# Performance work log

Measured on AMD Instinct MI355X. Metric: run time of the kernel, lower is better.

## Reference

```python
import jax, jax.numpy as jnp
import numpy as np

N = 100000   # n_node
D = 64       # emb_size
NNZ = 3200000
B, L = 64, 200
LAYERS = 2


def setup_inputs() -> dict:
    key = jax.random.key(0)
    ks = jax.random.split(key, 12)
    s = 1.0 / np.sqrt(D)  # reset_parameters uniform(-stdv, stdv)
    u = lambda k, shape: jax.random.uniform(k, shape, minval=-s, maxval=s, dtype=jnp.float32)
    return {
        "input": jax.random.randint(ks[0], (B, L), 0, N).astype(jnp.int32),
        "h_item_idx": jax.random.randint(ks[1], (2, NNZ), 0, N).astype(jnp.int32),
        "h_item_val": jax.random.uniform(ks[2], (NNZ,), dtype=jnp.float32),
        "h_user_idx": jax.random.randint(ks[3], (2, NNZ), 0, N).astype(jnp.int32),
        "h_user_val": jax.random.uniform(ks[4], (NNZ,), dtype=jnp.float32),
        "user_emb": u(ks[5], (N, D)),
        "w0": u(ks[6], (D, D)),
        "w1": u(ks[7], (D, D)),
        "b0": u(ks[8], (1, D)),
        "b1": u(ks[9], (1, D)),
        "att": u(ks[10], (1, D)),
        "att_m": u(ks[11], (D, D)),
    }


def _spmm(idx, val, x):
    # torch.sparse.mm(H, x) with H given as COO (rows=idx[0], cols=idx[1])
    gathered = val[:, None] * x[idx[1]]              # [nnz, D]
    return jax.ops.segment_sum(gathered, idx[0], num_segments=N)


def _l2norm(x):
    # F.normalize(x, p=2, dim=1), eps=1e-12
    n = jnp.maximum(jnp.linalg.norm(x, axis=1, keepdims=True), 1e-12)
    return x / n


def _structure_embed(h_item_idx, h_item_val, h_user_idx, h_user_val,
                     user_emb, w0, w1, b0, b1, att, att_m):
    # self_gating per channel (eval mode: no graph dropout)
    e2 = user_emb * jax.nn.sigmoid(user_emb @ w0 + b0)
    e3 = user_emb * jax.nn.sigmoid(user_emb @ w1 + b1)
    acc2, acc3 = e2, e3
    for _ in range(LAYERS):
        e2 = _spmm(h_item_idx, h_item_val, e2)
        acc2 = acc2 + _l2norm(e2)
        e3 = _spmm(h_user_idx, h_user_val, e3)
        acc3 = acc3 + _l2norm(e3)
    # channel attention over the two channel embeddings
    w_c2 = jnp.sum(att * (acc2 @ att_m), axis=1)     # [N]
    w_c3 = jnp.sum(att * (acc3 @ att_m), axis=1)     # [N]
    score = jax.nn.softmax(jnp.stack([w_c2, w_c3], axis=1), axis=-1)  # [N, 2]
    mixed = score[:, 0:1] * acc2 + score[:, 1:2] * acc3
    return mixed


def reference(input, h_item_idx, h_item_val, h_user_idx, h_user_val,
              user_emb, w0, w1, b0, b1, att, att_m):
    mask = input == 0                                 # [B, L]
    hg = _structure_embed(h_item_idx, h_item_val, h_user_idx, h_user_val,
                          user_emb, w0, w1, b0, b1, att, att_m)
    cas_seq_emb = hg[input]                           # [B, L, D]
    source_emb = cas_seq_emb[:, 0, :]                 # [B, D]
    # long-term attention: source query attends over the cascade sequence
    scores = jnp.einsum("bd,bld->bl", source_emb, cas_seq_emb) / np.sqrt(D)
    scores = jnp.where(mask, -1e9, scores)
    attw = jax.nn.softmax(scores, axis=-1)            # [B, L]
    L_cas_emb = attw[:, :, None] * cas_seq_emb        # [B, L, D]
    return (L_cas_emb, cas_seq_emb)
```

## Files before the change

### kernel.cpp

```cpp
#include <hip/hip_runtime.h>
#include <cstdint>
#include <cstddef>

typedef unsigned short ushort_t;

#define N_NODES 100000
#define D 64
#define NNZ 3200000
#define BB 64
#define LL 200
#define BSHIFT 7
#define BSIZE 128
#define NBUCK 782
#define CAP 4608
#define EPT 9
#define BM_WORDS 3200
#define BCHUNK 4096
#define BEPT 4

__device__ __forceinline__ float wave_sum(float x) {
#pragma unroll
  for (int o = 32; o; o >>= 1) x += __shfl_xor(x, o, 64);
  return x;
}
__device__ __forceinline__ float bf2f(uint32_t h) {
  return __uint_as_float(h << 16);
}
__device__ __forceinline__ uint32_t f2b(float f) {
  uint32_t u = __float_as_uint(f);
  return (u + 0x7FFFu + ((u >> 16) & 1u)) >> 16;
}

__global__ void mark_kernel(const int* __restrict__ input, uint32_t* __restrict__ bm,
                            int* __restrict__ list, int* __restrict__ nlist) {
  int t = blockIdx.x * 256 + threadIdx.x;
  if (t < BB * LL) {
    int i = input[t];
    uint32_t bit = 1u << (i & 31);
    uint32_t old = atomicOr(&bm[i >> 5], bit);
    if (!(old & bit)) {
      int p = atomicAdd(nlist, 1);
      list[p] = i;
    }
  }
}

__global__ __launch_bounds__(256) void gate_kernel(
    const float* __restrict__ u, const float* __restrict__ w0,
    const float* __restrict__ w1, const float* __restrict__ b0,
    const float* __restrict__ b1, float* __restrict__ e2, float* __restrict__ e3,
    ushort_t* __restrict__ h2, ushort_t* __restrict__ h3) {
  __shared__ float sw0[D * D];
  __shared__ float sw1[D * D];
  __shared__ float sb0[D], sb1[D];
  for (int t = threadIdx.x; t < D * D; t += 256) { sw0[t] = w0[t]; sw1[t] = w1[t]; }
  if (threadIdx.x < D) { sb0[threadIdx.x] = b0[threadIdx.x]; sb1[threadIdx.x] = b1[threadIdx.x]; }
  __syncthreads();
  int wave = (blockIdx.x * 256 + threadIdx.x) >> 6;
  int lane = threadIdx.x & 63;
  int nw = (gridDim.x * 256) >> 6;
  for (int i = wave; i < N_NODES; i += nw) {
    float uv = u[i * D + lane];
    float a0 = 0.f, a1 = 0.f;
#pragma unroll
    for (int k = 0; k < D; ++k) {
      float uk = __shfl(uv, k, 64);
      a0 = fmaf(uk, sw0[k * D + lane], a0);
      a1 = fmaf(uk, sw1[k * D + lane], a1);
    }
    a0 += sb0[lane];
    a1 += sb1[lane];
    float s0 = 1.f / (1.f + expf(-a0));
    float s1 = 1.f / (1.f + expf(-a1));
    float r2 = uv * s0, r3 = uv * s1;
    e2[i * D + lane] = r2;
    e3[i * D + lane] = r3;
    h2[i * D + lane] = (ushort_t)f2b(r2);
    h3[i * D + lane] = (ushort_t)f2b(r3);
  }
}

__global__ void init_cursor_kernel(uint32_t* __restrict__ gcursor) {
  int t = blockIdx.x * 256 + threadIdx.x;
  if (t < NBUCK) gcursor[t] = (uint32_t)t * CAP;
}

__global__ __launch_bounds__(1024) void bin_kernel(
    const int* __restrict__ dsts, const int* __restrict__ srcs,
    const float* __restrict__ val, uint32_t* __restrict__ gcursor,
    uint2* __restrict__ binned) {
  __shared__ uint2 sp[BCHUNK];
  __shared__ uint32_t hist[NBUCK];
  __shared__ uint32_t sst[NBUCK + 1];
  __shared__ uint32_t gbase[NBUCK];
  int base = blockIdx.x * BCHUNK;
  int tid = threadIdx.x;
  for (int t = tid; t < NBUCK; t += 1024) hist[t] = 0u;
  __syncthreads();
  int n = NNZ - base;
  if (n > BCHUNK) n = BCHUNK;
  uint32_t px[BEPT]; float pv[BEPT]; uint32_t pb[BEPT]; uint32_t pr[BEPT];
#pragma unroll
  for (int k = 0; k < BEPT; ++k) {
    int off = (k << 10) + tid;
    bool ok = off < n;
    int e = base + off;
    int d = ok ? dsts[e] : 0;
    int s = ok ? srcs[e] : 0;
    float v = ok ? val[e] : 0.f;
    uint32_t b = (uint32_t)d >> BSHIFT;
    pb[k] = ok ? b : 0xFFFFFFFFu;
    pr[k] = ok ? atomicAdd(&hist[b], 1u) : 0u;
    px[k] = (uint32_t)s | ((uint32_t)(d & (BSIZE - 1)) << 17);
    pv[k] = v;
  }
  __syncthreads();
  for (int t = tid; t < NBUCK; t += 1024) {
    uint32_t h = hist[t];
    gbase[t] = h ? atomicAdd(&gcursor[t], h) : 0u;
    sst[t + 1] = h;
  }
  if (tid == 0) sst[0] = 0u;
  __syncthreads();
  for (int o = 1; o < NBUCK; o <<= 1) {
    uint32_t t = 0u;
    if (tid < NBUCK && (int)(tid + 1) > o) t = sst[tid + 1 - o];
    __syncthreads();
    if (tid < NBUCK && (int)(tid + 1) > o) sst[tid + 1] += t;
    __syncthreads();
  }
#pragma unroll
  for (int k = 0; k < BEPT; ++k) {
    if (pb[k] != 0xFFFFFFFFu)
      sp[sst[pb[k]] + pr[k]] = make_uint2(px[k], __float_as_uint(pv[k]));
  }
  __syncthreads();
  for (int idx = tid; idx < n; idx += 1024) {
    int lo = 0, hi = NBUCK;
    while (hi - lo > 1) {
      int mid = (lo + hi) >> 1;
      if ((int)sst[mid] <= idx) lo = mid; else hi = mid;
    }
    uint32_t pos = gbase[lo] + ((uint32_t)idx - sst[lo]);
    if (pos < (uint32_t)(lo + 1) * CAP) {
      binned[pos] = sp[idx];
    }
  }
}

__global__ __launch_bounds__(512) void sortspmm_kernel(
    const uint32_t* __restrict__ gcursor, uint2* __restrict__ binned,
    const ushort_t* __restrict__ xin, ushort_t* __restrict__ xout,
    uint32_t* __restrict__ grow_start, uint32_t* __restrict__ grow_cnt) {
  __shared__ uint2 sp[CAP];
  __shared__ uint32_t hist[BSIZE];
  __shared__ uint32_t ssc[BSIZE];
  __shared__ uint32_t sst[BSIZE];
  int bucket = blockIdx.x, tid = threadIdx.x;
  int nodebase = bucket << BSHIFT;
  uint32_t cnt = gcursor[bucket] - (uint32_t)bucket * CAP;
  if (cnt > CAP) cnt = CAP;
  if (tid < BSIZE) hist[tid] = 0u;
  __syncthreads();
  uint2 pr[EPT]; uint32_t rk[EPT];
  const uint2* ep = binned + (size_t)bucket * CAP;
#pragma unroll
  for (int k = 0; k < EPT; ++k) {
    int e = (k << 9) + tid;
    if (e < (int)cnt) {
      pr[k] = ep[e];
      rk[k] = atomicAdd(&hist[pr[k].x >> 17], 1u);
    }
  }
  __syncthreads();
  if (tid < BSIZE) ssc[tid] = hist[tid];
  __syncthreads();
  for (int o = 1; o < BSIZE; o <<= 1) {
    uint32_t t = 0;
    if (tid < BSIZE && tid >= o) t = ssc[tid - o];
    __syncthreads();
    if (tid < BSIZE) ssc[tid] += t;
    __syncthreads();
  }
  if (tid < BSIZE) sst[tid] = ssc[tid] - hist[tid];
  __syncthreads();
#pragma unroll
  for (int k = 0; k < EPT; ++k) {
    int e = (k << 9) + tid;
    if (e < (int)cnt) sp[sst[pr[k].x >> 17] + rk[k]] = pr[k];
  }
  __syncthreads();
  for (int t = tid; t < (int)cnt; t += 512) binned[(size_t)bucket * CAP + t] = sp[t];
  int nvalid = N_NODES - nodebase;
  if (nvalid > BSIZE) nvalid = BSIZE;
  if (tid < nvalid) {
    grow_start[nodebase + tid] = (uint32_t)bucket * CAP + sst[tid];
    grow_cnt[nodebase + tid] = hist[tid];
  }
  int wave = tid >> 6, lane = tid & 63, g = lane >> 4, c = lane & 15;
  for (int r = wave; r < nvalid; r += 8) {
    uint32_t rc = hist[r], s0 = sst[r];
    float ax = 0.f, ay = 0.f, az = 0.f, aw = 0.f;
    for (uint32_t j0 = 0; j0 < rc; j0 += 32) {
      uint2 pk[8];
#pragma unroll
      for (int k = 0; k < 8; ++k) {
        uint32_t e = j0 + (uint32_t)g + (uint32_t)(k << 2);
        pk[k] = (e < rc) ? sp[s0 + e] : make_uint2(0u, 0u);
      }
      uint2 qk[8];
#pragma unroll
      for (int k = 0; k < 8; ++k) {
        uint32_t src = pk[k].x & 0x1FFFFu;
        qk[k] = ((const uint2*)(xin + (size_t)src * D))[c];
      }
#pragma unroll
      for (int k = 0; k < 8; ++k) {
        float v = __uint_as_float(pk[k].y);
        ax = fmaf(v, bf2f(qk[k].x & 0xFFFFu), ax);
        ay = fmaf(v, bf2f(qk[k].x >> 16), ay);
        az = fmaf(v, bf2f(qk[k].y & 0xFFFFu), az);
        aw = fmaf(v, bf2f(qk[k].y >> 16), aw);
      }
    }
#pragma unroll
    for (int o = 16; o <= 32; o <<= 1) {
      ax += __shfl_xor(ax, o, 64); ay += __shfl_xor(ay, o, 64);
      az += __shfl_xor(az, o, 64); aw += __shfl_xor(aw, o, 64);
    }
    if (g == 0) {
      uint32_t lo = f2b(ax) | (f2b(ay) << 16);
      uint32_t hi = f2b(az) | (f2b(aw) << 16);
      ((uint2*)(xout + (size_t)(nodebase + r) * D))[c] = make_uint2(lo, hi);
    }
  }
}

__global__ __launch_bounds__(256) void listspmm_kernel(
    const uint32_t* __restrict__ grow_start, const uint32_t* __restrict__ grow_cnt,
    const uint2* __restrict__ pairs, const ushort_t* __restrict__ xin,
    float* __restrict__ xout, const int* __restrict__ list, const int* __restrict__ nlist) {
  int wave = (blockIdx.x * 256 + threadIdx.x) >> 6;
  int lane = threadIdx.x & 63;
  int nw = (gridDim.x * 256) >> 6;
  int g = lane >> 4, c = lane & 15;
  int n = nlist[0];
  for (int ii = wave; ii < n; ii += nw) {
    int i = list[ii];
    uint32_t rc = grow_cnt[i];
    uint32_t base = grow_start[i];
    float ax = 0.f, ay = 0.f, az = 0.f, aw = 0.f;
    for (uint32_t j0 = 0; j0 < rc; j0 += 32) {
      uint2 pk[8];
#pragma unroll
      for (int k = 0; k < 8; ++k) {
        uint32_t e = j0 + (uint32_t)g + (uint32_t)(k << 2);
        pk[k] = (e < rc) ? pairs[base + e] : make_uint2(0u, 0u);
      }
      uint2 qk[8];
#pragma unroll
      for (int k = 0; k < 8; ++k) {
        uint32_t src = pk[k].x & 0x1FFFFu;
        qk[k] = ((const uint2*)(xin + (size_t)src * D))[c];
      }
#pragma unroll
      for (int k = 0; k < 8; ++k) {
        float v = __uint_as_float(pk[k].y);
        ax = fmaf(v, bf2f(qk[k].x & 0xFFFFu), ax);
        ay = fmaf(v, bf2f(qk[k].x >> 16), ay);
        az = fmaf(v, bf2f(qk[k].y & 0xFFFFu), az);
        aw = fmaf(v, bf2f(qk[k].y >> 16), aw);
      }
    }
#pragma unroll
    for (int o = 16; o <= 32; o <<= 1) {
      ax += __shfl_xor(ax, o, 64); ay += __shfl_xor(ay, o, 64);
      az += __shfl_xor(az, o, 64); aw += __shfl_xor(aw, o, 64);
    }
    if (g == 0)
      ((float4*)(xout + (size_t)i * D))[c] = make_float4(ax, ay, az, aw);
  }
}

__global__ __launch_bounds__(256) void final_kernel(
    const int* __restrict__ input,
    const float* __restrict__ e20, const ushort_t* __restrict__ h21, const float* __restrict__ e22,
    const float* __restrict__ e30, const ushort_t* __restrict__ h31, const float* __restrict__ e32,
    const float* __restrict__ att, const float* __restrict__ att_m,
    float* __restrict__ out_Lcas, float* __restrict__ out_cas) {
  __shared__ float cas[LL * D];
  __shared__ float sv[D];
  __shared__ float sscore[LL];
  __shared__ float red[8];
  int b = blockIdx.x, tid = threadIdx.x;
  if (tid < D) {
    float a = 0.f;
#pragma unroll
    for (int j = 0; j < D; ++j) a = fmaf(att_m[tid * D + j], att[j], a);
    sv[tid] = a;
  }
  __syncthreads();
  int wv = tid >> 6, lane = tid & 63;
  float svl = sv[lane];
  for (int l = wv; l < LL; l += 4) {
    int i = input[b * LL + l];
    size_t o = (size_t)i * D + lane;
    float v20 = e20[o], v22 = e22[o];
    float v30 = e30[o], v32 = e32[o];
    float v21 = bf2f((uint32_t)h21[o]);
    float v31 = bf2f((uint32_t)h31[o]);
    float n21 = fmaxf(sqrtf(wave_sum(v21 * v21)), 1e-12f);
    float n22 = fmaxf(sqrtf(wave_sum(v22 * v22)), 1e-12f);
    float n31 = fmaxf(sqrtf(wave_sum(v31 * v31)), 1e-12f);
    float n32 = fmaxf(sqrtf(wave_sum(v32 * v32)), 1e-12f);
    float a2 = v20 + v21 / n21 + v22 / n22;
    float a3 = v30 + v31 / n31 + v32 / n32;
    float w2 = wave_sum(a2 * svl);
    float w3 = wave_sum(a3 * svl);
    float mx = fmaxf(w2, w3);
    float ex2 = expf(w2 - mx), ex3 = expf(w3 - mx);
    float inv = 1.f / (ex2 + ex3);
    float mix = (ex2 * a2 + ex3 * a3) * inv;
    cas[l * D + lane] = mix;
    out_cas[(size_t)(b * LL + l) * D + lane] = mix;
  }
  __syncthreads();
  for (int l = wv; l < LL; l += 4) {
    float s = wave_sum(cas[lane] * cas[l * D + lane]) * 0.125f;
    int iv = input[b * LL + l];
    s = (iv == 0) ? -1e9f : s;
    if (lane == 0) sscore[l] = s;
  }
  __syncthreads();
  float m = -INFINITY;
  for (int l = tid; l < LL; l += 256) m = fmaxf(m, sscore[l]);
#pragma unroll
  for (int o = 32; o; o >>= 1) m = fmaxf(m, __shfl_xor(m, o, 64));
  if (lane == 0) red[wv] = m;
  __syncthreads();
  m = fmaxf(fmaxf(red[0], red[1]), fmaxf(red[2], red[3]));
  float sum = 0.f;
  for (int l = tid; l < LL; l += 256) sum += expf(sscore[l] - m);
  sum = wave_sum(sum);
  if (lane == 0) red[4 + wv] = sum;
  __syncthreads();
  float inv = 1.f / (red[4] + red[5] + red[6] + red[7]);
  for (int l = tid; l < LL; l += 256) sscore[l] = expf(sscore[l] - m) * inv;
  __syncthreads();
  for (int t = tid; t < LL * D; t += 256)
    out_Lcas[(size_t)b * LL * D + t] = sscore[t >> 6] * cas[t];
}

extern "C" void kernel_launch(void* const* d_in, const int* in_sizes, int n_in,
                              void* d_out, int out_size, void* d_ws, size_t ws_size,
                              hipStream_t stream) {
  const int* input = (const int*)d_in[0];
  const int* h_item_idx = (const int*)d_in[1];
  const float* h_item_val = (const float*)d_in[2];
  const int* h_user_idx = (const int*)d_in[3];
  const float* h_user_val = (const float*)d_in[4];
  const float* user_emb = (const float*)d_in[5];
  const float* w0 = (const float*)d_in[6];
  const float* w1 = (const float*)d_in[7];
  const float* b0 = (const float*)d_in[8];
  const float* b1 = (const float*)d_in[9];
  const float* att = (const float*)d_in[10];
  const float* att_m = (const float*)d_in[11];

  float* out = (float*)d_out;
  float* out_Lcas = out;
  float* out_cas = out + (size_t)BB * LL * D;

  const size_t ND = (size_t)N_NODES * D;
  char* ws = (char*)d_ws;
  float* e20 = (float*)ws; ws += ND * 4;
  float* e30 = (float*)ws; ws += ND * 4;
  float* e22 = (float*)ws; ws += ND * 4;
  float* e32 = (float*)ws; ws += ND * 4;
  ushort_t* h20 = (ushort_t*)ws; ws += ND * 2;
  ushort_t* h30 = (ushort_t*)ws; ws += ND * 2;
  ushort_t* h21 = (ushort_t*)ws; ws += ND * 2;
  ushort_t* h31 = (ushort_t*)ws; ws += ND * 2;
  uint2* binned = (uint2*)ws; ws += (size_t)NBUCK * CAP * 8;
  uint32_t* gcursor = (uint32_t*)ws; ws += (size_t)((NBUCK + 63) & ~63) * 4;
  uint32_t* bitmap = (uint32_t*)ws; ws += (size_t)BM_WORDS * 4;
  uint32_t* grow_start = (uint32_t*)ws; ws += (size_t)N_NODES * 4;
  uint32_t* grow_cnt = (uint32_t*)ws; ws += (size_t)N_NODES * 4;
  int* list = (int*)ws; ws += (size_t)(BB * LL) * 4;
  int* nlist = (int*)ws; ws += 64;

  const int* item_dst = h_item_idx;
  const int* item_src = h_item_idx + NNZ;
  const int* user_dst = h_user_idx;
  const int* user_src = h_user_idx + NNZ;

  const int BIN_BLOCKS = (NNZ + BCHUNK - 1) / BCHUNK;

  hipMemsetAsync(bitmap, 0, (size_t)BM_WORDS * 4, stream);
  hipMemsetAsync(nlist, 0, 64, stream);
  mark_kernel<<<(BB * LL + 255) / 256, 256, 0, stream>>>(input, bitmap, list, nlist);

  gate_kernel<<<2048, 256, 0, stream>>>(user_emb, w0, w1, b0, b1, e20, e30, h20, h30);

  init_cursor_kernel<<<(NBUCK + 255) / 256, 256, 0, stream>>>(gcursor);
  bin_kernel<<<BIN_BLOCKS, 1024, 0, stream>>>(item_dst, item_src, h_item_val, gcursor, binned);
  sortspmm_kernel<<<NBUCK, 512, 0, stream>>>(gcursor, binned, h20, h21, grow_start, grow_cnt);
  listspmm_kernel<<<3200, 256, 0, stream>>>(grow_start, grow_cnt, binned, h21, e22, list, nlist);

  init_cursor_kernel<<<(NBUCK + 255) / 256, 256, 0, stream>>>(gcursor);
  bin_kernel<<<BIN_BLOCKS, 1024, 0, stream>>>(user_dst, user_src, h_user_val, gcursor, binned);
  sortspmm_kernel<<<NBUCK, 512, 0, stream>>>(gcursor, binned, h30, h31, grow_start, grow_cnt);
  listspmm_kernel<<<3200, 256, 0, stream>>>(grow_start, grow_cnt, binned, h31, e32, list, nlist);

  final_kernel<<<BB, 256, 0, stream>>>(input, e20, h21, e22, e30, h31, e32,
                                       att, att_m, out_Lcas, out_cas);
}
```

Before: 548.7 us.

## Drop fp32 gate outputs, pack bf16 weights, process four rows per wave

The gate kernel no longer writes the fp32 e20/e30 arrays, and the final kernel reads the bf16 h20/h30 copies in their place. This removes about 51 MB of global writes. The two weight matrices are packed as bf16 pairs in a single shared array, and each wave now handles four rows so each shared-memory weight load is reused across rows, with the grid halved. Using bf16 for the layer-0 term in the final accumulation lowers precision slightly.

```diff
diff --git a/kernel.cpp b/kernel.cpp
--- a/kernel.cpp
+++ b/kernel.cpp
@@ -48,35 +48,50 @@
 __global__ __launch_bounds__(256) void gate_kernel(
     const float* __restrict__ u, const float* __restrict__ w0,
     const float* __restrict__ w1, const float* __restrict__ b0,
-    const float* __restrict__ b1, float* __restrict__ e2, float* __restrict__ e3,
+    const float* __restrict__ b1,
     ushort_t* __restrict__ h2, ushort_t* __restrict__ h3) {
-  __shared__ float sw0[D * D];
-  __shared__ float sw1[D * D];
+  __shared__ uint32_t sw01[D * D];
   __shared__ float sb0[D], sb1[D];
-  for (int t = threadIdx.x; t < D * D; t += 256) { sw0[t] = w0[t]; sw1[t] = w1[t]; }
+  for (int t = threadIdx.x; t < D * D; t += 256)
+    sw01[t] = f2b(w0[t]) | (f2b(w1[t]) << 16);
   if (threadIdx.x < D) { sb0[threadIdx.x] = b0[threadIdx.x]; sb1[threadIdx.x] = b1[threadIdx.x]; }
   __syncthreads();
   int wave = (blockIdx.x * 256 + threadIdx.x) >> 6;
   int lane = threadIdx.x & 63;
   int nw = (gridDim.x * 256) >> 6;
-  for (int i = wave; i < N_NODES; i += nw) {
-    float uv = u[i * D + lane];
-    float a0 = 0.f, a1 = 0.f;
-#pragma unroll
+  const int NT = N_NODES >> 2;
+  for (int t = wave; t < NT; t += nw) {
+    int row = t << 2;
+    float uv0 = u[(size_t)(row + 0) * D + lane];
+    float uv1 = u[(size_t)(row + 1) * D + lane];
+    float uv2 = u[(size_t)(row + 2) * D + lane];
+    float uv3 = u[(size_t)(row + 3) * D + lane];
+    float a00 = 0.f, a01 = 0.f, a02 = 0.f, a03 = 0.f;
+    float a10 = 0.f, a11 = 0.f, a12 = 0.f, a13 = 0.f;
+#pragma unroll 16
     for (int k = 0; k < D; ++k) {
-      float uk = __shfl(uv, k, 64);
-      a0 = fmaf(uk, sw0[k * D + lane], a0);
-      a1 = fmaf(uk, sw1[k * D + lane], a1);
-    }
-    a0 += sb0[lane];
-    a1 += sb1[lane];
-    float s0 = 1.f / (1.f + expf(-a0));
-    float s1 = 1.f / (1.f + expf(-a1));
-    float r2 = uv * s0, r3 = uv * s1;
-    e2[i * D + lane] = r2;
-    e3[i * D + lane] = r3;
-    h2[i * D + lane] = (ushort_t)f2b(r2);
-    h3[i * D + lane] = (ushort_t)f2b(r3);
+      uint32_t wp = sw01[k * D + lane];
+      float wa = bf2f(wp & 0xFFFFu);
+      float wb = bf2f(wp >> 16);
+      float u0 = __shfl(uv0, k, 64);
+      float u1 = __shfl(uv1, k, 64);
+      float u2 = __shfl(uv2, k, 64);
+      float u3 = __shfl(uv3, k, 64);
+      a00 = fmaf(u0, wa, a00); a10 = fmaf(u0, wb, a10);
+      a01 = fmaf(u1, wa, a01); a11 = fmaf(u1, wb, a11);
+      a02 = fmaf(u2, wa, a02); a12 = fmaf(u2, wb, a12);
+      a03 = fmaf(u3, wa, a03); a13 = fmaf(u3, wb, a13);
+    }
+    float bb0 = sb0[lane], bb1 = sb1[lane];
+    float s;
+    s = 1.f / (1.f + expf(-(a00 + bb0))); h2[(size_t)(row + 0) * D + lane] = (ushort_t)f2b(uv0 * s);
+    s = 1.f / (1.f + expf(-(a01 + bb0))); h2[(size_t)(row + 1) * D + lane] = (ushort_t)f2b(uv1 * s);
+    s = 1.f / (1.f + expf(-(a02 + bb0))); h2[(size_t)(row + 2) * D + lane] = (ushort_t)f2b(uv2 * s);
+    s = 1.f / (1.f + expf(-(a03 + bb0))); h2[(size_t)(row + 3) * D + lane] = (ushort_t)f2b(uv3 * s);
+    s = 1.f / (1.f + expf(-(a10 + bb1))); h3[(size_t)(row + 0) * D + lane] = (ushort_t)f2b(uv0 * s);
+    s = 1.f / (1.f + expf(-(a11 + bb1))); h3[(size_t)(row + 1) * D + lane] = (ushort_t)f2b(uv1 * s);
+    s = 1.f / (1.f + expf(-(a12 + bb1))); h3[(size_t)(row + 2) * D + lane] = (ushort_t)f2b(uv2 * s);
+    s = 1.f / (1.f + expf(-(a13 + bb1))); h3[(size_t)(row + 3) * D + lane] = (ushort_t)f2b(uv3 * s);
   }
 }
 
@@ -284,8 +299,8 @@
 
 __global__ __launch_bounds__(256) void final_kernel(
     const int* __restrict__ input,
-    const float* __restrict__ e20, const ushort_t* __restrict__ h21, const float* __restrict__ e22,
-    const float* __restrict__ e30, const ushort_t* __restrict__ h31, const float* __restrict__ e32,
+    const ushort_t* __restrict__ h20, const ushort_t* __restrict__ h21, const float* __restrict__ e22,
+    const ushort_t* __restrict__ h30, const ushort_t* __restrict__ h31, const float* __restrict__ e32,
     const float* __restrict__ att, const float* __restrict__ att_m,
     float* __restrict__ out_Lcas, float* __restrict__ out_cas) {
   __shared__ float cas[LL * D];
@@ -305,8 +320,8 @@
   for (int l = wv; l < LL; l += 4) {
     int i = input[b * LL + l];
     size_t o = (size_t)i * D + lane;
-    float v20 = e20[o], v22 = e22[o];
-    float v30 = e30[o], v32 = e32[o];
+    float v20 = bf2f((uint32_t)h20[o]), v22 = e22[o];
+    float v30 = bf2f((uint32_t)h30[o]), v32 = e32[o];
     float v21 = bf2f((uint32_t)h21[o]);
     float v31 = bf2f((uint32_t)h31[o]);
     float n21 = fmaxf(sqrtf(wave_sum(v21 * v21)), 1e-12f);
@@ -373,8 +388,6 @@
 
   const size_t ND = (size_t)N_NODES * D;
   char* ws = (char*)d_ws;
-  float* e20 = (float*)ws; ws += ND * 4;
-  float* e30 = (float*)ws; ws += ND * 4;
   float* e22 = (float*)ws; ws += ND * 4;
   float* e32 = (float*)ws; ws += ND * 4;
   ushort_t* h20 = (ushort_t*)ws; ws += ND * 2;
@@ -400,7 +413,7 @@
   hipMemsetAsync(nlist, 0, 64, stream);
   mark_kernel<<<(BB * LL + 255) / 256, 256, 0, stream>>>(input, bitmap, list, nlist);
 
-  gate_kernel<<<2048, 256, 0, stream>>>(user_emb, w0, w1, b0, b1, e20, e30, h20, h30);
+  gate_kernel<<<1024, 256, 0, stream>>>(user_emb, w0, w1, b0, b1, h20, h30);
 
   init_cursor_kernel<<<(NBUCK + 255) / 256, 256, 0, stream>>>(gcursor);
   bin_kernel<<<BIN_BLOCKS, 1024, 0, stream>>>(item_dst, item_src, h_item_val, gcursor, binned);
@@ -412,6 +425,6 @@
   sortspmm_kernel<<<NBUCK, 512, 0, stream>>>(gcursor, binned, h30, h31, grow_start, grow_cnt);
   listspmm_kernel<<<3200, 256, 0, stream>>>(grow_start, grow_cnt, binned, h31, e32, list, nlist);
 
-  final_kernel<<<BB, 256, 0, stream>>>(input, e20, h21, e22, e30, h31, e32,
+  final_kernel<<<BB, 256, 0, stream>>>(input, h20, h21, e22, h30, h31, e32,
                                        att, att_m, out_Lcas, out_cas);
 }
```

New measurement: 545.0 us. About the same (-0.7%).
